# Optimization experiments

Measured on AMD Instinct MI355X. Metric: run time of the kernel, lower is better.

## Reference

```python
import jax, jax.numpy as jnp
import numpy as np

L, H, E, D, FF, V, CTX = 8, 16, 1024, 64, 4096, 2048, 2048
B, T = 4, 1024


def _ln(x, g, b, eps=1e-5):
    mu = x.mean(-1, keepdims=True)
    var = ((x - mu) ** 2).mean(-1, keepdims=True)
    return (x - mu) * jax.lax.rsqrt(var + eps) * g + b


def setup_inputs() -> dict:
    key = jax.random.key(0)
    ks = jax.random.split(key, 12)
    s = 0.02
    return {
        "tokens": jax.random.randint(ks[0], (B, T), 0, V),
        "tok_emb": jax.random.normal(ks[1], (V, E), jnp.float32) * s,
        "pos_emb": jax.random.normal(ks[2], (CTX, E), jnp.float32) * s,
        "Wq": jax.random.normal(ks[3], (L, H, E, D), jnp.float32) * s,
        "Wk": jax.random.normal(ks[4], (L, H, E, D), jnp.float32) * s,
        "Wv": jax.random.normal(ks[5], (L, H, E, D), jnp.float32) * s,
        "Wo": jax.random.normal(ks[6], (L, H * D, E), jnp.float32) * s,
        "bo": jnp.zeros((L, E), jnp.float32),
        "ln1_g": jnp.ones((L, E), jnp.float32),
        "ln1_b": jnp.zeros((L, E), jnp.float32),
        "ln2_g": jnp.ones((L, E), jnp.float32),
        "ln2_b": jnp.zeros((L, E), jnp.float32),
        "W1": jax.random.normal(ks[7], (L, E, FF), jnp.float32) * s,
        "b1": jnp.zeros((L, FF), jnp.float32),
        "W2": jax.random.normal(ks[8], (L, FF, E), jnp.float32) * s,
        "b2": jnp.zeros((L, E), jnp.float32),
        "lnf_g": jnp.ones((E,), jnp.float32),
        "lnf_b": jnp.zeros((E,), jnp.float32),
        "Wlm": jax.random.normal(ks[9], (E, V), jnp.float32) * s,
        "blm": jnp.zeros((V,), jnp.float32),
    }


def reference(tokens, tok_emb, pos_emb, Wq, Wk, Wv, Wo, bo, ln1_g, ln1_b,
              ln2_g, ln2_b, W1, b1, W2, b2, lnf_g, lnf_b, Wlm, blm):
    # NOTE: original indexes pos_embd with token ids (pos_embd(x.int()))
    x = tok_emb[tokens] + pos_emb[tokens]  # [B,T,E]
    t = x.shape[1]
    causal = jnp.tril(jnp.ones((t, t), bool))
    scale = 1.0 / jnp.sqrt(jnp.float32(D))
    for l in range(L):
        x = _ln(x, ln1_g[l], ln1_b[l])
        q = jnp.einsum('bte,hed->bhtd', x, Wq[l])
        k = jnp.einsum('bte,hed->bhtd', x, Wk[l])
        v = jnp.einsum('bte,hed->bhtd', x, Wv[l])
        scores = jnp.einsum('bhtd,bhsd->bhts', q, k) * scale
        scores = jnp.where(causal, scores, -jnp.inf)
        att = jax.nn.softmax(scores, axis=-1)
        o = jnp.einsum('bhts,bhsd->bhtd', att, v)
        o = o.transpose(0, 2, 1, 3).reshape(x.shape[0], t, H * D)
        x = x + o @ Wo[l] + bo[l]
        x = _ln(x, ln2_g[l], ln2_b[l])
        x = x + jax.nn.relu(x @ W1[l] + b1[l]) @ W2[l] + b2[l]
    x = _ln(x, lnf_g, lnf_b)
    return x @ Wlm + blm
```

## Files before the change

### kernel.cpp

```cpp
#include <hip/hip_runtime.h>
#include <hip/hip_bf16.h>

#define LAYERS 8
#define H_ 16
#define E_ 1024
#define D_ 64
#define FF_ 4096
#define V_ 2048
#define B_ 4
#define T_ 1024
#define MTOK (B_*T_)

typedef __bf16 bf16x8_t __attribute__((ext_vector_type(8)));
typedef float f32x4_t __attribute__((ext_vector_type(4)));
typedef __hip_bfloat16 bf16_t;

__device__ __forceinline__ bf16_t f2b(float f) { return __float2bfloat16(f); }

__global__ void embed_kernel(const int* __restrict__ tokens,
                             const float* __restrict__ te,
                             const float* __restrict__ pe,
                             float* __restrict__ x) {
  int row = blockIdx.x;
  int tok = tokens[row];
  const float4* a = (const float4*)(te + (size_t)tok * E_);
  const float4* p = (const float4*)(pe + (size_t)tok * E_);
  float4* o = (float4*)(x + (size_t)row * E_);
  int t = threadIdx.x;
  float4 va = a[t], vp = p[t];
  o[t] = make_float4(va.x + vp.x, va.y + vp.y, va.z + vp.z, va.w + vp.w);
}

__global__ __launch_bounds__(256) void ln_kernel(float* __restrict__ x,
                                                 bf16_t* __restrict__ xb,
                                                 const float* __restrict__ g,
                                                 const float* __restrict__ b) {
  int row = blockIdx.x, tid = threadIdx.x;
  float* xr = x + (size_t)row * E_;
  float4 v = ((const float4*)xr)[tid];
  float s  = v.x + v.y + v.z + v.w;
  float sq = v.x*v.x + v.y*v.y + v.z*v.z + v.w*v.w;
  for (int off = 32; off; off >>= 1) {
    s  += __shfl_xor(s, off, 64);
    sq += __shfl_xor(sq, off, 64);
  }
  __shared__ float2 wred[4];
  if ((tid & 63) == 0) wred[tid >> 6] = make_float2(s, sq);
  __syncthreads();
  float2 w0 = wred[0], w1 = wred[1], w2 = wred[2], w3 = wred[3];
  float S = w0.x + w1.x + w2.x + w3.x, SQ = w0.y + w1.y + w2.y + w3.y;
  float mean = S * (1.0f / E_);
  float var  = SQ * (1.0f / E_) - mean * mean;
  float inv = rsqrtf(var + 1e-5f);
  float4 gv = ((const float4*)g)[tid];
  float4 bv = ((const float4*)b)[tid];
  float o0 = (v.x - mean) * inv * gv.x + bv.x;
  float o1 = (v.y - mean) * inv * gv.y + bv.y;
  float o2 = (v.z - mean) * inv * gv.z + bv.z;
  float o3 = (v.w - mean) * inv * gv.w + bv.w;
  ((float4*)xr)[tid] = make_float4(o0, o1, o2, o3);
  bf16_t* xo = xb + (size_t)row * E_ + tid * 4;
  xo[0] = f2b(o0); xo[1] = f2b(o1); xo[2] = f2b(o2); xo[3] = f2b(o3);
}

__global__ void transpose_kernel(const float* __restrict__ in, bf16_t* __restrict__ out,
                                 int R, int C) {
  __shared__ float tile[32][33];
  int z = blockIdx.z;
  const float* ib = in + (size_t)z * R * C;
  bf16_t* ob = out + (size_t)z * R * C;
  int r0 = blockIdx.y * 32, c0 = blockIdx.x * 32;
  int tx = threadIdx.x, ty = threadIdx.y;
  for (int i = 0; i < 4; i++)
    tile[ty + i * 8][tx] = ib[(size_t)(r0 + ty + i * 8) * C + (c0 + tx)];
  __syncthreads();
  for (int i = 0; i < 4; i++)
    ob[(size_t)(c0 + ty + i * 8) * R + (r0 + tx)] = f2b(tile[tx][ty + i * 8]);
}

#define BK 32

enum { MODE_F32 = 0, MODE_BF16 = 1, MODE_QKV = 2 };

__device__ __forceinline__ void gload16(const bf16_t* g, bf16_t* l) {
  __builtin_amdgcn_global_load_lds((const __attribute__((address_space(1))) void*)g,
                                   (__attribute__((address_space(3))) void*)l, 16, 0, 0);
}

__device__ __forceinline__ int xcd_swz(int flat, int nwg) {
  int q = nwg >> 3, r = nwg & 7;
  int xcd = flat & 7, idx = flat >> 3;
  return (xcd < r ? xcd * (q + 1) : r * (q + 1) + (xcd - r) * q) + idx;
}

template <int BM, int BN, int MODE>
__global__ __launch_bounds__(256) void gemm97_kernel(
    const bf16_t* __restrict__ A, long long sAz, int lda,
    const bf16_t* __restrict__ Bt, long long sBz, int ldb,
    void* __restrict__ C, long long sCz,
    const float* __restrict__ bias,
    const float* __restrict__ resid,
    int M, int N, int K, float alpha, int relu) {
  constexpr int FR = BM / 32, FC = BN / 32;
  constexpr int A_ISS = BM / 64, B_ISS = BN / 64;
  __shared__ __align__(16) bf16_t As[2][BM * BK];
  __shared__ __align__(16) bf16_t Bs[2][BN * BK];
  int tid = threadIdx.x;
  int z = blockIdx.z;
  int nwg = gridDim.x * gridDim.y;
  int flat = xcd_swz(blockIdx.y * gridDim.x + blockIdx.x, nwg);
  int m0 = (flat / gridDim.x) * BM, n0 = (flat % gridDim.x) * BN;
  const bf16_t* Ab = A + (size_t)z * sAz + (size_t)m0 * lda;
  const bf16_t* Bb = Bt + (size_t)z * sBz + (size_t)n0 * ldb;
  int lane = tid & 63, wave = tid >> 6;
  int wr = (wave >> 1) * (BM / 2), wc = (wave & 1) * (BN / 2);
  int lr = lane & 15, lk = (lane >> 4) * 8;
  int srow = tid >> 2;
  int scol = (tid & 3) * 8;

  f32x4_t acc[FR][FC];
  for (int i = 0; i < FR; i++)
    for (int j = 0; j < FC; j++)
      acc[i][j] = (f32x4_t){0.f, 0.f, 0.f, 0.f};

  auto stage = [&](int buf, int k0) {
#pragma unroll
    for (int i = 0; i < A_ISS; i++)
      gload16(Ab + (size_t)(i * 64 + srow) * lda + k0 + scol, &As[buf][i * 2048 + wave * 512]);
#pragma unroll
    for (int i = 0; i < B_ISS; i++)
      gload16(Bb + (size_t)(i * 64 + srow) * ldb + k0 + scol, &Bs[buf][i * 2048 + wave * 512]);
  };

  int nk = K / BK;
  stage(0, 0);
  __syncthreads();
  int cur = 0;
  for (int kt = 0; kt < nk; ++kt) {
    if (kt + 1 < nk) stage(cur ^ 1, (kt + 1) * BK);
    bf16x8_t af[FR], bfv[FC];
#pragma unroll
    for (int i = 0; i < FR; i++)
      af[i] = *(const bf16x8_t*)(&As[cur][(wr + i * 16 + lr) * BK + lk]);
#pragma unroll
    for (int j = 0; j < FC; j++)
      bfv[j] = *(const bf16x8_t*)(&Bs[cur][(wc + j * 16 + lr) * BK + lk]);
#pragma unroll
    for (int i = 0; i < FR; i++)
#pragma unroll
      for (int j = 0; j < FC; j++)
        acc[i][j] = __builtin_amdgcn_mfma_f32_16x16x32_bf16(af[i], bfv[j], acc[i][j], 0, 0, 0);
    __syncthreads();
    cur ^= 1;
  }

#pragma unroll
  for (int i = 0; i < FR; i++)
#pragma unroll
    for (int j = 0; j < FC; j++) {
      f32x4_t v = acc[i][j];
      int n = n0 + wc + j * 16 + lr;
      int mb = m0 + wr + i * 16 + (lane >> 4) * 4;
#pragma unroll
      for (int r = 0; r < 4; r++) {
        int m = mb + r;
        float val = v[r] * alpha;
        if (bias) val += bias[n];
        if (relu) val = fmaxf(val, 0.f);
        if (MODE == MODE_F32) {
          size_t idx = (size_t)z * sCz + (size_t)m * N + n;
          ((float*)C)[idx] = val + (resid ? resid[idx] : 0.f);
        } else if (MODE == MODE_BF16) {
          size_t idx = (size_t)z * sCz + (size_t)m * N + n;
          ((bf16_t*)C)[idx] = f2b(val);
        } else {
          int sect = n >> 10, hd = n & 1023, h = hd >> 6, d = hd & 63;
          int b = m >> 10, t = m & 1023;
          size_t base = (size_t)sect * ((size_t)B_ * H_ * T_ * D_);
          size_t idx = base + ((size_t)(b * H_ + h) << 16) +
                       (sect == 2 ? (size_t)((d << 10) + t) : (size_t)((t << 6) + d));
          ((bf16_t*)C)[idx] = f2b(val);
        }
      }
    }
}

template <int NS>
__global__ __launch_bounds__(256) void splitk_reduce_kernel(const float* __restrict__ p,
                                                            float* __restrict__ x,
                                                            const float* __restrict__ bias) {
  size_t i = (size_t)blockIdx.x * 256 + threadIdx.x;
  float4 acc = ((float4*)x)[i];
  int n4 = (int)(i & (E_ / 4 - 1));
  float4 bv = ((const float4*)bias)[n4];
  acc.x += bv.x; acc.y += bv.y; acc.z += bv.z; acc.w += bv.w;
#pragma unroll
  for (int s = 0; s < NS; s++) {
    float4 a = ((const float4*)p)[i + (size_t)s * ((size_t)MTOK * E_ / 4)];
    acc.x += a.x; acc.y += a.y; acc.z += a.z; acc.w += a.w;
  }
  ((float4*)x)[i] = acc;
}

#define KPAD 72

__global__ __launch_bounds__(256) void flash_kernel(
    const bf16_t* __restrict__ q,
    const bf16_t* __restrict__ kk,
    const bf16_t* __restrict__ vt,
    bf16_t* __restrict__ o) {
  __shared__ __align__(16) bf16_t Ks[64 * KPAD];
  __shared__ __align__(16) bf16_t Vs[64 * KPAD];
  __shared__ __align__(16) bf16_t Ps[4][16 * KPAD];
  int bid = blockIdx.x;
  int qi = 15 - (bid >> 6);
  int bh = bid & 63;
  int b = bh >> 4, h = bh & 15;
  const bf16_t* qb = q + ((size_t)bh << 16);
  const bf16_t* kb = kk + ((size_t)bh << 16);
  const bf16_t* vb = vt + ((size_t)bh << 16);
  int tid = threadIdx.x, lane = tid & 63, wave = tid >> 6;
  int lr = lane & 15, lg = lane >> 4;
  int qbase = qi * 64;

  bf16x8_t qf[2];
  {
    const bf16_t* qrow = qb + (size_t)(qbase + wave * 16 + lr) * D_ + lg * 8;
    qf[0] = *(const bf16x8_t*)(qrow);
    qf[1] = *(const bf16x8_t*)(qrow + 32);
  }

  float m_r[4], l_r[4];
  f32x4_t oc[4];
#pragma unroll
  for (int r = 0; r < 4; r++) { m_r[r] = -1e30f; l_r[r] = 0.f; }
#pragma unroll
  for (int j = 0; j < 4; j++) oc[j] = (f32x4_t){0.f, 0.f, 0.f, 0.f};

  int srow = tid >> 2, scol = (tid & 3) * 16;

  bf16x8_t k0, k1, v0, v1;
  {
    const bf16_t* kg = kb + (size_t)srow * D_ + scol;
    k0 = *(const bf16x8_t*)kg;
    k1 = *(const bf16x8_t*)(kg + 8);
    const bf16_t* vg = vb + (size_t)srow * T_ + scol;
    v0 = *(const bf16x8_t*)vg;
    v1 = *(const bf16x8_t*)(vg + 8);
  }

  for (int s = 0; s <= qi; s++) {
    __syncthreads();
    *(bf16x8_t*)(&Ks[srow * KPAD + scol]) = k0;
    *(bf16x8_t*)(&Ks[srow * KPAD + scol + 8]) = k1;
    *(bf16x8_t*)(&Vs[srow * KPAD + scol]) = v0;
    *(bf16x8_t*)(&Vs[srow * KPAD + scol + 8]) = v1;
    __syncthreads();

    if (s < qi) {
      int kv1 = (s + 1) * 64;
      const bf16_t* kg = kb + (size_t)(kv1 + srow) * D_ + scol;
      k0 = *(const bf16x8_t*)kg;
      k1 = *(const bf16x8_t*)(kg + 8);
      const bf16_t* vg = vb + (size_t)srow * T_ + kv1 + scol;
      v0 = *(const bf16x8_t*)vg;
      v1 = *(const bf16x8_t*)(vg + 8);
    }

    int kv0 = s * 64;
    f32x4_t sc[4];
#pragma unroll
    for (int j = 0; j < 4; j++) {
      f32x4_t a = (f32x4_t){0.f, 0.f, 0.f, 0.f};
      bf16x8_t b0 = *(const bf16x8_t*)(&Ks[(j * 16 + lr) * KPAD + lg * 8]);
      bf16x8_t b1 = *(const bf16x8_t*)(&Ks[(j * 16 + lr) * KPAD + lg * 8 + 32]);
      a = __builtin_amdgcn_mfma_f32_16x16x32_bf16(qf[0], b0, a, 0, 0, 0);
      a = __builtin_amdgcn_mfma_f32_16x16x32_bf16(qf[1], b1, a, 0, 0, 0);
      sc[j] = a;
    }
    if (s == qi) {
#pragma unroll
      for (int j = 0; j < 4; j++)
#pragma unroll
        for (int r = 0; r < 4; r++) {
          int kvp = kv0 + j * 16 + lr;
          int qp  = qbase + wave * 16 + lg * 4 + r;
          sc[j][r] = (kvp <= qp) ? sc[j][r] * 0.125f : -1e30f;
        }
    } else {
#pragma unroll
      for (int j = 0; j < 4; j++)
#pragma unroll
        for (int r = 0; r < 4; r++) sc[j][r] *= 0.125f;
    }

    float ex[4];
#pragma unroll
    for (int r = 0; r < 4; r++) {
      float v = fmaxf(fmaxf(sc[0][r], sc[1][r]), fmaxf(sc[2][r], sc[3][r]));
      v = fmaxf(v, __shfl_xor(v, 1, 64));
      v = fmaxf(v, __shfl_xor(v, 2, 64));
      v = fmaxf(v, __shfl_xor(v, 4, 64));
      v = fmaxf(v, __shfl_xor(v, 8, 64));
      float mn = fmaxf(m_r[r], v);
      ex[r] = __expf(m_r[r] - mn);
      m_r[r] = mn;
      l_r[r] *= ex[r];
    }
#pragma unroll
    for (int j = 0; j < 4; j++)
#pragma unroll
      for (int r = 0; r < 4; r++) {
        float p = __expf(sc[j][r] - m_r[r]);
        l_r[r] += p;
        Ps[wave][(lg * 4 + r) * KPAD + j * 16 + lr] = f2b(p);
      }

#pragma unroll
    for (int j = 0; j < 4; j++)
#pragma unroll
      for (int r = 0; r < 4; r++) oc[j][r] *= ex[r];

    bf16x8_t pa0 = *(const bf16x8_t*)(&Ps[wave][lr * KPAD + lg * 8]);
    bf16x8_t pa1 = *(const bf16x8_t*)(&Ps[wave][lr * KPAD + lg * 8 + 32]);
#pragma unroll
    for (int j = 0; j < 4; j++) {
      bf16x8_t vb0 = *(const bf16x8_t*)(&Vs[(j * 16 + lr) * KPAD + lg * 8]);
      bf16x8_t vb1 = *(const bf16x8_t*)(&Vs[(j * 16 + lr) * KPAD + lg * 8 + 32]);
      oc[j] = __builtin_amdgcn_mfma_f32_16x16x32_bf16(pa0, vb0, oc[j], 0, 0, 0);
      oc[j] = __builtin_amdgcn_mfma_f32_16x16x32_bf16(pa1, vb1, oc[j], 0, 0, 0);
    }
  }

#pragma unroll
  for (int r = 0; r < 4; r++) {
    float v = l_r[r];
    v += __shfl_xor(v, 1, 64);
    v += __shfl_xor(v, 2, 64);
    v += __shfl_xor(v, 4, 64);
    v += __shfl_xor(v, 8, 64);
    l_r[r] = 1.f / v;
  }
  bf16_t* ob = o + ((size_t)(b * T_ + qbase + wave * 16)) * (H_ * D_) + h * D_;
#pragma unroll
  for (int j = 0; j < 4; j++)
#pragma unroll
    for (int r = 0; r < 4; r++) {
      int qrow = lg * 4 + r;
      ob[(size_t)qrow * (H_ * D_) + j * 16 + lr] = f2b(oc[j][r] * l_r[r]);
    }
}

extern "C" void kernel_launch(void* const* d_in, const int* in_sizes, int n_in,
                              void* d_out, int out_size, void* d_ws, size_t ws_size,
                              hipStream_t stream) {
  (void)in_sizes; (void)n_in; (void)out_size;
  const int*   tokens = (const int*)d_in[0];
  const float* tok_emb = (const float*)d_in[1];
  const float* pos_emb = (const float*)d_in[2];
  const float* Wq = (const float*)d_in[3];
  const float* Wk = (const float*)d_in[4];
  const float* Wv = (const float*)d_in[5];
  const float* Wo = (const float*)d_in[6];
  const float* bo = (const float*)d_in[7];
  const float* ln1_g = (const float*)d_in[8];
  const float* ln1_b = (const float*)d_in[9];
  const float* ln2_g = (const float*)d_in[10];
  const float* ln2_b = (const float*)d_in[11];
  const float* W1 = (const float*)d_in[12];
  const float* b1 = (const float*)d_in[13];
  const float* W2 = (const float*)d_in[14];
  const float* b2 = (const float*)d_in[15];
  const float* lnf_g = (const float*)d_in[16];
  const float* lnf_b = (const float*)d_in[17];
  const float* Wlm = (const float*)d_in[18];
  const float* blm = (const float*)d_in[19];

  char* w = (char*)d_ws;
  size_t off = 0;
  auto alloc = [&](size_t bytes) { void* p = (void*)(w + off); off += (bytes + 255) & ~(size_t)255; return p; };
  float*  x    = (float*)alloc((size_t)MTOK * E_ * 4);
  bf16_t* xb   = (bf16_t*)alloc((size_t)MTOK * E_ * 2);
  bf16_t* q    = (bf16_t*)alloc((size_t)B_ * H_ * T_ * D_ * 2);
  bf16_t* kk   = (bf16_t*)alloc((size_t)B_ * H_ * T_ * D_ * 2);
  bf16_t* vt   = (bf16_t*)alloc((size_t)B_ * H_ * T_ * D_ * 2);
  bf16_t* o    = (bf16_t*)alloc((size_t)MTOK * E_ * 2);
  bf16_t* h1   = (bf16_t*)alloc((size_t)MTOK * FF_ * 2);
  bf16_t* WqkvT = (bf16_t*)alloc((size_t)3 * E_ * H_ * D_ * 2);
  bf16_t* WoT  = (bf16_t*)alloc((size_t)E_ * H_ * D_ * 2);
  bf16_t* W1T  = (bf16_t*)alloc((size_t)E_ * FF_ * 2);
  bf16_t* W2T  = (bf16_t*)alloc((size_t)E_ * FF_ * 2);
  bf16_t* WlmT = (bf16_t*)alloc((size_t)E_ * V_ * 2);
  size_t pk_bytes = (size_t)4 * MTOK * E_ * 4;
  bool do_splitk = (ws_size > off + pk_bytes + (1 << 20));
  float* p4 = do_splitk ? (float*)alloc(pk_bytes) : nullptr;

  embed_kernel<<<MTOK, 256, 0, stream>>>(tokens, tok_emb, pos_emb, x);
  transpose_kernel<<<dim3(V_ / 32, E_ / 32, 1), dim3(32, 8), 0, stream>>>(Wlm, WlmT, E_, V_);

  for (int l = 0; l < LAYERS; l++) {
    ln_kernel<<<MTOK, 256, 0, stream>>>(x, xb, ln1_g + l * E_, ln1_b + l * E_);

    transpose_kernel<<<dim3(D_ / 32, E_ / 32, H_), dim3(32, 8), 0, stream>>>(
        Wq + (size_t)l * H_ * E_ * D_, WqkvT, E_, D_);
    transpose_kernel<<<dim3(D_ / 32, E_ / 32, H_), dim3(32, 8), 0, stream>>>(
        Wk + (size_t)l * H_ * E_ * D_, WqkvT + (size_t)E_ * H_ * D_, E_, D_);
    transpose_kernel<<<dim3(D_ / 32, E_ / 32, H_), dim3(32, 8), 0, stream>>>(
        Wv + (size_t)l * H_ * E_ * D_, WqkvT + (size_t)2 * E_ * H_ * D_, E_, D_);
    transpose_kernel<<<dim3(E_ / 32, (H_ * D_) / 32, 1), dim3(32, 8), 0, stream>>>(
        Wo + (size_t)l * H_ * D_ * E_, WoT, H_ * D_, E_);
    transpose_kernel<<<dim3(FF_ / 32, E_ / 32, 1), dim3(32, 8), 0, stream>>>(
        W1 + (size_t)l * E_ * FF_, W1T, E_, FF_);
    transpose_kernel<<<dim3(E_ / 32, FF_ / 32, 1), dim3(32, 8), 0, stream>>>(
        W2 + (size_t)l * FF_ * E_, W2T, FF_, E_);

    gemm97_kernel<128, 128, MODE_QKV><<<dim3(24, 32, 1), 256, 0, stream>>>(
        xb, 0, E_, WqkvT, 0, E_, q, 0, nullptr, nullptr, MTOK, 3 * H_ * D_, E_, 1.f, 0);

    flash_kernel<<<1024, 256, 0, stream>>>(q, kk, vt, o);

    if (do_splitk) {
      gemm97_kernel<128, 128, MODE_F32><<<dim3(8, 32, 2), 256, 0, stream>>>(
          o, 512, H_ * D_, WoT, 512, H_ * D_, p4, (long long)MTOK * E_,
          nullptr, nullptr, MTOK, E_, (H_ * D_) / 2, 1.f, 0);
      splitk_reduce_kernel<2><<<MTOK * E_ / 1024, 256, 0, stream>>>(p4, x, bo + l * E_);
    } else {
      gemm97_kernel<128, 128, MODE_F32><<<dim3(8, 32, 1), 256, 0, stream>>>(
          o, 0, H_ * D_, WoT, 0, H_ * D_, x, 0, bo + l * E_, x, MTOK, E_, H_ * D_, 1.f, 0);
    }

    ln_kernel<<<MTOK, 256, 0, stream>>>(x, xb, ln2_g + l * E_, ln2_b + l * E_);

    gemm97_kernel<128, 128, MODE_BF16><<<dim3(32, 32, 1), 256, 0, stream>>>(
        xb, 0, E_, W1T, 0, E_, h1, 0, b1 + l * FF_, nullptr, MTOK, FF_, E_, 1.f, 1);
    if (do_splitk) {
      gemm97_kernel<128, 128, MODE_F32><<<dim3(8, 32, 4), 256, 0, stream>>>(
          h1, 1024, FF_, W2T, 1024, FF_, p4, (long long)MTOK * E_,
          nullptr, nullptr, MTOK, E_, FF_ / 4, 1.f, 0);
      splitk_reduce_kernel<4><<<MTOK * E_ / 1024, 256, 0, stream>>>(p4, x, b2 + l * E_);
    } else {
      gemm97_kernel<128, 128, MODE_F32><<<dim3(8, 32, 1), 256, 0, stream>>>(
          h1, 0, FF_, W2T, 0, FF_, x, 0, b2 + l * E_, x, MTOK, E_, FF_, 1.f, 0);
    }
  }

  ln_kernel<<<MTOK, 256, 0, stream>>>(x, xb, lnf_g, lnf_b);
  gemm97_kernel<128, 128, MODE_F32><<<dim3(16, 32, 1), 256, 0, stream>>>(
      xb, 0, E_, WlmT, 0, E_, d_out, 0, blm, nullptr, MTOK, V_, E_, 1.f, 0);
}
```

Before: 2.391 ms.

## Replace 128x128 GEMM with 256-row, 512-thread, BK=64 prefetch-two GEMM kernel

Replaces the 128x128/BK=32 GEMM with a kernel using 256-row tiles, 512 threads and BK=64. Operand tiles are stored as 16x32 fragment chunks so each lane reads its MFMA fragment directly. The k-loop keeps two tiles in flight, waits on vmcnt counters instead of a full sync before each compute, and raises wave priority around MFMAs. Split-K is dropped for the Wo projection and reduced from 4 to 2 for W2, which trades fewer reduction passes for fewer blocks (fewer CTAs may underfill the GPU) and larger LDS use per block.

```diff
diff --git a/kernel.cpp b/kernel.cpp
--- a/kernel.cpp
+++ b/kernel.cpp
@@ -78,8 +78,6 @@
     ob[(size_t)(c0 + ty + i * 8) * R + (r0 + tx)] = f2b(tile[tx][ty + i * 8]);
 }
 
-#define BK 32
-
 enum { MODE_F32 = 0, MODE_BF16 = 1, MODE_QKV = 2 };
 
 __device__ __forceinline__ void gload16(const bf16_t* g, bf16_t* l) {
@@ -93,85 +91,104 @@
   return (xcd < r ? xcd * (q + 1) : r * (q + 1) + (xcd - r) * q) + idx;
 }
 
-template <int BM, int BN, int MODE>
-__global__ __launch_bounds__(256) void gemm97_kernel(
-    const bf16_t* __restrict__ A, long long sAz, int lda,
-    const bf16_t* __restrict__ Bt, long long sBz, int ldb,
+template <int BN, int MODE>
+__global__ __launch_bounds__(512, 2) void gemm256_kernel(
+    const bf16_t* __restrict__ A, int lda,
+    const bf16_t* __restrict__ Bt, int ldb,
     void* __restrict__ C, long long sCz,
     const float* __restrict__ bias,
     const float* __restrict__ resid,
-    int M, int N, int K, float alpha, int relu) {
-  constexpr int FR = BM / 32, FC = BN / 32;
-  constexpr int A_ISS = BM / 64, B_ISS = BN / 64;
-  __shared__ __align__(16) bf16_t As[2][BM * BK];
-  __shared__ __align__(16) bf16_t Bs[2][BN * BK];
-  int tid = threadIdx.x;
+    int M, int N, int kspan, int relu) {
+  constexpr int WN = BN / 64;
+  constexpr int WM = 8 / WN;
+  constexpr int MF = 16 / WM;
+  constexpr int ACH = 4;
+  constexpr int BCH = BN / 64;
+  constexpr int LPS = ACH + BCH;
+  __shared__ __align__(16) bf16_t As[2][256 * 64];
+  __shared__ __align__(16) bf16_t Bs[2][BN * 64];
+  int tid = threadIdx.x, lane = tid & 63, wave = tid >> 6;
+  int wm = wave / WN, wn = wave % WN;
   int z = blockIdx.z;
   int nwg = gridDim.x * gridDim.y;
   int flat = xcd_swz(blockIdx.y * gridDim.x + blockIdx.x, nwg);
-  int m0 = (flat / gridDim.x) * BM, n0 = (flat % gridDim.x) * BN;
-  const bf16_t* Ab = A + (size_t)z * sAz + (size_t)m0 * lda;
-  const bf16_t* Bb = Bt + (size_t)z * sBz + (size_t)n0 * ldb;
-  int lane = tid & 63, wave = tid >> 6;
-  int wr = (wave >> 1) * (BM / 2), wc = (wave & 1) * (BN / 2);
-  int lr = lane & 15, lk = (lane >> 4) * 8;
-  int srow = tid >> 2;
-  int scol = (tid & 3) * 8;
-
-  f32x4_t acc[FR][FC];
-  for (int i = 0; i < FR; i++)
-    for (int j = 0; j < FC; j++)
+  int m0 = (flat / gridDim.x) * 256, n0 = (flat % gridDim.x) * BN;
+  const bf16_t* Ab = A + (size_t)m0 * lda + (size_t)z * kspan;
+  const bf16_t* Bb = Bt + (size_t)n0 * ldb + (size_t)z * kspan;
+  int sr = lane & 15, sc = (lane >> 4) * 8;
+
+  f32x4_t acc[MF][4];
+#pragma unroll
+  for (int i = 0; i < MF; i++)
+#pragma unroll
+    for (int j = 0; j < 4; j++)
       acc[i][j] = (f32x4_t){0.f, 0.f, 0.f, 0.f};
 
-  auto stage = [&](int buf, int k0) {
-#pragma unroll
-    for (int i = 0; i < A_ISS; i++)
-      gload16(Ab + (size_t)(i * 64 + srow) * lda + k0 + scol, &As[buf][i * 2048 + wave * 512]);
-#pragma unroll
-    for (int i = 0; i < B_ISS; i++)
-      gload16(Bb + (size_t)(i * 64 + srow) * ldb + k0 + scol, &Bs[buf][i * 2048 + wave * 512]);
+  auto stage = [&](int buf, int kt) {
+    int kg = kt * 64;
+#pragma unroll
+    for (int ch = 0; ch < ACH; ch++) {
+      int sub = wave * ACH + ch;
+      gload16(Ab + (size_t)((sub >> 1) * 16 + sr) * lda + kg + (sub & 1) * 32 + sc,
+              &As[buf][sub * 512]);
+    }
+#pragma unroll
+    for (int ch = 0; ch < BCH; ch++) {
+      int sub = wave * BCH + ch;
+      gload16(Bb + (size_t)((sub >> 1) * 16 + sr) * ldb + kg + (sub & 1) * 32 + sc,
+              &Bs[buf][sub * 512]);
+    }
   };
 
-  int nk = K / BK;
+  int nk = kspan / 64;
   stage(0, 0);
-  __syncthreads();
+  stage(1, 1);
   int cur = 0;
   for (int kt = 0; kt < nk; ++kt) {
-    if (kt + 1 < nk) stage(cur ^ 1, (kt + 1) * BK);
-    bf16x8_t af[FR], bfv[FC];
-#pragma unroll
-    for (int i = 0; i < FR; i++)
-      af[i] = *(const bf16x8_t*)(&As[cur][(wr + i * 16 + lr) * BK + lk]);
-#pragma unroll
-    for (int j = 0; j < FC; j++)
-      bfv[j] = *(const bf16x8_t*)(&Bs[cur][(wc + j * 16 + lr) * BK + lk]);
-#pragma unroll
-    for (int i = 0; i < FR; i++)
-#pragma unroll
-      for (int j = 0; j < FC; j++)
-        acc[i][j] = __builtin_amdgcn_mfma_f32_16x16x32_bf16(af[i], bfv[j], acc[i][j], 0, 0, 0);
-    __syncthreads();
+    if (kt + 1 < nk) { asm volatile("s_waitcnt vmcnt(%0)" :: "n"(LPS) : "memory"); }
+    else             { asm volatile("s_waitcnt vmcnt(0)" ::: "memory"); }
+    __builtin_amdgcn_s_barrier();
+#pragma unroll
+    for (int ks = 0; ks < 2; ks++) {
+      bf16x8_t af[MF], bfv[4];
+#pragma unroll
+      for (int i = 0; i < MF; i++)
+        af[i] = *(const bf16x8_t*)(&As[cur][((wm * MF + i) * 2 + ks) * 512 + lane * 8]);
+#pragma unroll
+      for (int j = 0; j < 4; j++)
+        bfv[j] = *(const bf16x8_t*)(&Bs[cur][((wn * 4 + j) * 2 + ks) * 512 + lane * 8]);
+      __builtin_amdgcn_s_setprio(1);
+#pragma unroll
+      for (int i = 0; i < MF; i++)
+#pragma unroll
+        for (int j = 0; j < 4; j++)
+          acc[i][j] = __builtin_amdgcn_mfma_f32_16x16x32_bf16(af[i], bfv[j], acc[i][j], 0, 0, 0);
+      __builtin_amdgcn_s_setprio(0);
+    }
+    __builtin_amdgcn_sched_barrier(0);
+    __builtin_amdgcn_s_barrier();
+    if (kt + 2 < nk) stage(cur, kt + 2);
     cur ^= 1;
   }
 
 #pragma unroll
-  for (int i = 0; i < FR; i++)
-#pragma unroll
-    for (int j = 0; j < FC; j++) {
+  for (int i = 0; i < MF; i++)
+#pragma unroll
+    for (int j = 0; j < 4; j++) {
       f32x4_t v = acc[i][j];
-      int n = n0 + wc + j * 16 + lr;
-      int mb = m0 + wr + i * 16 + (lane >> 4) * 4;
+      int n = n0 + wn * 64 + j * 16 + (lane & 15);
+      int mb = m0 + wm * (256 / WM) + i * 16 + (lane >> 4) * 4;
 #pragma unroll
       for (int r = 0; r < 4; r++) {
         int m = mb + r;
-        float val = v[r] * alpha;
+        float val = v[r];
         if (bias) val += bias[n];
         if (relu) val = fmaxf(val, 0.f);
         if (MODE == MODE_F32) {
           size_t idx = (size_t)z * sCz + (size_t)m * N + n;
           ((float*)C)[idx] = val + (resid ? resid[idx] : 0.f);
         } else if (MODE == MODE_BF16) {
-          size_t idx = (size_t)z * sCz + (size_t)m * N + n;
+          size_t idx = (size_t)m * N + n;
           ((bf16_t*)C)[idx] = f2b(val);
         } else {
           int sect = n >> 10, hd = n & 1023, h = hd >> 6, d = hd & 63;
@@ -354,7 +371,7 @@
 extern "C" void kernel_launch(void* const* d_in, const int* in_sizes, int n_in,
                               void* d_out, int out_size, void* d_ws, size_t ws_size,
                               hipStream_t stream) {
-  (void)in_sizes; (void)n_in; (void)out_size;
+  (void)in_sizes; (void)n_in; (void)out_size; (void)ws_size;
   const int*   tokens = (const int*)d_in[0];
   const float* tok_emb = (const float*)d_in[1];
   const float* pos_emb = (const float*)d_in[2];
@@ -391,9 +408,7 @@
   bf16_t* W1T  = (bf16_t*)alloc((size_t)E_ * FF_ * 2);
   bf16_t* W2T  = (bf16_t*)alloc((size_t)E_ * FF_ * 2);
   bf16_t* WlmT = (bf16_t*)alloc((size_t)E_ * V_ * 2);
-  size_t pk_bytes = (size_t)4 * MTOK * E_ * 4;
-  bool do_splitk = (ws_size > off + pk_bytes + (1 << 20));
-  float* p4 = do_splitk ? (float*)alloc(pk_bytes) : nullptr;
+  float*  p2   = (float*)alloc((size_t)2 * MTOK * E_ * 4);
 
   embed_kernel<<<MTOK, 256, 0, stream>>>(tokens, tok_emb, pos_emb, x);
   transpose_kernel<<<dim3(V_ / 32, E_ / 32, 1), dim3(32, 8), 0, stream>>>(Wlm, WlmT, E_, V_);
@@ -414,37 +429,24 @@
     transpose_kernel<<<dim3(E_ / 32, FF_ / 32, 1), dim3(32, 8), 0, stream>>>(
         W2 + (size_t)l * FF_ * E_, W2T, FF_, E_);
 
-    gemm97_kernel<128, 128, MODE_QKV><<<dim3(24, 32, 1), 256, 0, stream>>>(
-        xb, 0, E_, WqkvT, 0, E_, q, 0, nullptr, nullptr, MTOK, 3 * H_ * D_, E_, 1.f, 0);
+    gemm256_kernel<256, MODE_QKV><<<dim3(12, 16, 1), 512, 0, stream>>>(
+        xb, E_, WqkvT, E_, q, 0, nullptr, nullptr, MTOK, 3 * H_ * D_, E_, 0);
 
     flash_kernel<<<1024, 256, 0, stream>>>(q, kk, vt, o);
 
-    if (do_splitk) {
-      gemm97_kernel<128, 128, MODE_F32><<<dim3(8, 32, 2), 256, 0, stream>>>(
-          o, 512, H_ * D_, WoT, 512, H_ * D_, p4, (long long)MTOK * E_,
-          nullptr, nullptr, MTOK, E_, (H_ * D_) / 2, 1.f, 0);
-      splitk_reduce_kernel<2><<<MTOK * E_ / 1024, 256, 0, stream>>>(p4, x, bo + l * E_);
-    } else {
-      gemm97_kernel<128, 128, MODE_F32><<<dim3(8, 32, 1), 256, 0, stream>>>(
-          o, 0, H_ * D_, WoT, 0, H_ * D_, x, 0, bo + l * E_, x, MTOK, E_, H_ * D_, 1.f, 0);
-    }
+    gemm256_kernel<128, MODE_F32><<<dim3(8, 16, 1), 512, 0, stream>>>(
+        o, H_ * D_, WoT, H_ * D_, x, 0, bo + l * E_, x, MTOK, E_, H_ * D_, 0);
 
     ln_kernel<<<MTOK, 256, 0, stream>>>(x, xb, ln2_g + l * E_, ln2_b + l * E_);
 
-    gemm97_kernel<128, 128, MODE_BF16><<<dim3(32, 32, 1), 256, 0, stream>>>(
-        xb, 0, E_, W1T, 0, E_, h1, 0, b1 + l * FF_, nullptr, MTOK, FF_, E_, 1.f, 1);
-    if (do_splitk) {
-      gemm97_kernel<128, 128, MODE_F32><<<dim3(8, 32, 4), 256, 0, stream>>>(
-          h1, 1024, FF_, W2T, 1024, FF_, p4, (long long)MTOK * E_,
-          nullptr, nullptr, MTOK, E_, FF_ / 4, 1.f, 0);
-      splitk_reduce_kernel<4><<<MTOK * E_ / 1024, 256, 0, stream>>>(p4, x, b2 + l * E_);
-    } else {
-      gemm97_kernel<128, 128, MODE_F32><<<dim3(8, 32, 1), 256, 0, stream>>>(
-          h1, 0, FF_, W2T, 0, FF_, x, 0, b2 + l * E_, x, MTOK, E_, FF_, 1.f, 0);
-    }
+    gemm256_kernel<256, MODE_BF16><<<dim3(16, 16, 1), 512, 0, stream>>>(
+        xb, E_, W1T, E_, h1, 0, b1 + l * FF_, nullptr, MTOK, FF_, E_, 1);
+    gemm256_kernel<128, MODE_F32><<<dim3(8, 16, 2), 512, 0, stream>>>(
+        h1, FF_, W2T, FF_, p2, (long long)MTOK * E_, nullptr, nullptr, MTOK, E_, FF_ / 2, 0);
+    splitk_reduce_kernel<2><<<MTOK * E_ / 1024, 256, 0, stream>>>(p2, x, b2 + l * E_);
   }
 
   ln_kernel<<<MTOK, 256, 0, stream>>>(x, xb, lnf_g, lnf_b);
-  gemm97_kernel<128, 128, MODE_F32><<<dim3(16, 32, 1), 256, 0, stream>>>(
-      xb, 0, E_, WlmT, 0, E_, d_out, 0, blm, nullptr, MTOK, V_, E_, 1.f, 0);
-}
+  gemm256_kernel<128, MODE_F32><<<dim3(16, 16, 1), 512, 0, stream>>>(
+      xb, E_, WlmT, E_, d_out, 0, blm, nullptr, MTOK, V_, E_, 0);
+}
```

New measurement: 2.889 ms. +20.8%, slower.

## Keep residual stream in bf16 and fuse Wo residual into GEMM epilogue

Applied to the files above, without the earlier changes.

Stores the residual activation stream as bf16 instead of fp32. Layernorm now reads bf16 and writes only a bf16 output, and the Wo projection adds its residual in a new bf16 epilogue, which removes that split-K pass and its reduce kernel. The W2 GEMM now uses 2-way split-K with bf16 partials instead of 4-way fp32. The goal is less memory traffic and fewer launches, at the cost of rounding the residual and the partial sums to bf16, which risks accuracy.

```diff
diff --git a/kernel.cpp b/kernel.cpp
--- a/kernel.cpp
+++ b/kernel.cpp
@@ -12,6 +12,7 @@
 #define MTOK (B_*T_)
 
 typedef __bf16 bf16x8_t __attribute__((ext_vector_type(8)));
+typedef __bf16 bf16x4_t __attribute__((ext_vector_type(4)));
 typedef float f32x4_t __attribute__((ext_vector_type(4)));
 typedef __hip_bfloat16 bf16_t;
 
@@ -20,26 +21,27 @@
 __global__ void embed_kernel(const int* __restrict__ tokens,
                              const float* __restrict__ te,
                              const float* __restrict__ pe,
-                             float* __restrict__ x) {
+                             bf16_t* __restrict__ x) {
   int row = blockIdx.x;
   int tok = tokens[row];
-  const float4* a = (const float4*)(te + (size_t)tok * E_);
-  const float4* p = (const float4*)(pe + (size_t)tok * E_);
-  float4* o = (float4*)(x + (size_t)row * E_);
   int t = threadIdx.x;
-  float4 va = a[t], vp = p[t];
-  o[t] = make_float4(va.x + vp.x, va.y + vp.y, va.z + vp.z, va.w + vp.w);
-}
-
-__global__ __launch_bounds__(256) void ln_kernel(float* __restrict__ x,
-                                                 bf16_t* __restrict__ xb,
+  float4 va = ((const float4*)(te + (size_t)tok * E_))[t];
+  float4 vp = ((const float4*)(pe + (size_t)tok * E_))[t];
+  bf16x4_t o;
+  o[0] = (__bf16)(va.x + vp.x); o[1] = (__bf16)(va.y + vp.y);
+  o[2] = (__bf16)(va.z + vp.z); o[3] = (__bf16)(va.w + vp.w);
+  ((bf16x4_t*)(x + (size_t)row * E_))[t] = o;
+}
+
+__global__ __launch_bounds__(256) void ln_kernel(const bf16_t* __restrict__ xin,
+                                                 bf16_t* __restrict__ xout,
                                                  const float* __restrict__ g,
                                                  const float* __restrict__ b) {
   int row = blockIdx.x, tid = threadIdx.x;
-  float* xr = x + (size_t)row * E_;
-  float4 v = ((const float4*)xr)[tid];
-  float s  = v.x + v.y + v.z + v.w;
-  float sq = v.x*v.x + v.y*v.y + v.z*v.z + v.w*v.w;
+  bf16x4_t v4 = ((const bf16x4_t*)(xin + (size_t)row * E_))[tid];
+  float v0 = (float)v4[0], v1 = (float)v4[1], v2 = (float)v4[2], v3 = (float)v4[3];
+  float s  = v0 + v1 + v2 + v3;
+  float sq = v0*v0 + v1*v1 + v2*v2 + v3*v3;
   for (int off = 32; off; off >>= 1) {
     s  += __shfl_xor(s, off, 64);
     sq += __shfl_xor(sq, off, 64);
@@ -54,13 +56,12 @@
   float inv = rsqrtf(var + 1e-5f);
   float4 gv = ((const float4*)g)[tid];
   float4 bv = ((const float4*)b)[tid];
-  float o0 = (v.x - mean) * inv * gv.x + bv.x;
-  float o1 = (v.y - mean) * inv * gv.y + bv.y;
-  float o2 = (v.z - mean) * inv * gv.z + bv.z;
-  float o3 = (v.w - mean) * inv * gv.w + bv.w;
-  ((float4*)xr)[tid] = make_float4(o0, o1, o2, o3);
-  bf16_t* xo = xb + (size_t)row * E_ + tid * 4;
-  xo[0] = f2b(o0); xo[1] = f2b(o1); xo[2] = f2b(o2); xo[3] = f2b(o3);
+  bf16x4_t o;
+  o[0] = (__bf16)((v0 - mean) * inv * gv.x + bv.x);
+  o[1] = (__bf16)((v1 - mean) * inv * gv.y + bv.y);
+  o[2] = (__bf16)((v2 - mean) * inv * gv.z + bv.z);
+  o[3] = (__bf16)((v3 - mean) * inv * gv.w + bv.w);
+  ((bf16x4_t*)(xout + (size_t)row * E_))[tid] = o;
 }
 
 __global__ void transpose_kernel(const float* __restrict__ in, bf16_t* __restrict__ out,
@@ -80,7 +81,7 @@
 
 #define BK 32
 
-enum { MODE_F32 = 0, MODE_BF16 = 1, MODE_QKV = 2 };
+enum { MODE_F32 = 0, MODE_BF16 = 1, MODE_QKV = 2, MODE_BF16R = 3 };
 
 __device__ __forceinline__ void gload16(const bf16_t* g, bf16_t* l) {
   __builtin_amdgcn_global_load_lds((const __attribute__((address_space(1))) void*)g,
@@ -99,8 +100,8 @@
     const bf16_t* __restrict__ Bt, long long sBz, int ldb,
     void* __restrict__ C, long long sCz,
     const float* __restrict__ bias,
-    const float* __restrict__ resid,
-    int M, int N, int K, float alpha, int relu) {
+    const void* __restrict__ resid,
+    int M, int N, int K, int relu) {
   constexpr int FR = BM / 32, FC = BN / 32;
   constexpr int A_ISS = BM / 64, B_ISS = BN / 64;
   __shared__ __align__(16) bf16_t As[2][BM * BK];
@@ -164,14 +165,18 @@
 #pragma unroll
       for (int r = 0; r < 4; r++) {
         int m = mb + r;
-        float val = v[r] * alpha;
+        float val = v[r];
         if (bias) val += bias[n];
         if (relu) val = fmaxf(val, 0.f);
         if (MODE == MODE_F32) {
           size_t idx = (size_t)z * sCz + (size_t)m * N + n;
-          ((float*)C)[idx] = val + (resid ? resid[idx] : 0.f);
+          ((float*)C)[idx] = val + (resid ? ((const float*)resid)[idx] : 0.f);
         } else if (MODE == MODE_BF16) {
           size_t idx = (size_t)z * sCz + (size_t)m * N + n;
+          ((bf16_t*)C)[idx] = f2b(val);
+        } else if (MODE == MODE_BF16R) {
+          size_t idx = (size_t)m * N + n;
+          val += __bfloat162float(((const bf16_t*)resid)[idx]);
           ((bf16_t*)C)[idx] = f2b(val);
         } else {
           int sect = n >> 10, hd = n & 1023, h = hd >> 6, d = hd & 63;
@@ -186,20 +191,26 @@
 }
 
 template <int NS>
-__global__ __launch_bounds__(256) void splitk_reduce_kernel(const float* __restrict__ p,
-                                                            float* __restrict__ x,
+__global__ __launch_bounds__(256) void splitk_reduce_kernel(const bf16_t* __restrict__ p,
+                                                            const bf16_t* __restrict__ t,
+                                                            bf16_t* __restrict__ r,
                                                             const float* __restrict__ bias) {
   size_t i = (size_t)blockIdx.x * 256 + threadIdx.x;
-  float4 acc = ((float4*)x)[i];
-  int n4 = (int)(i & (E_ / 4 - 1));
-  float4 bv = ((const float4*)bias)[n4];
-  acc.x += bv.x; acc.y += bv.y; acc.z += bv.z; acc.w += bv.w;
+  bf16x8_t tv = ((const bf16x8_t*)t)[i];
+  int base = (int)((i * 8) & (E_ - 1));
+  float acc[8];
+#pragma unroll
+  for (int j = 0; j < 8; j++) acc[j] = (float)tv[j] + bias[base + j];
 #pragma unroll
   for (int s = 0; s < NS; s++) {
-    float4 a = ((const float4*)p)[i + (size_t)s * ((size_t)MTOK * E_ / 4)];
-    acc.x += a.x; acc.y += a.y; acc.z += a.z; acc.w += a.w;
-  }
-  ((float4*)x)[i] = acc;
+    bf16x8_t pv = ((const bf16x8_t*)p)[i + (size_t)s * ((size_t)MTOK * E_ / 8)];
+#pragma unroll
+    for (int j = 0; j < 8; j++) acc[j] += (float)pv[j];
+  }
+  bf16x8_t ov;
+#pragma unroll
+  for (int j = 0; j < 8; j++) ov[j] = (__bf16)acc[j];
+  ((bf16x8_t*)r)[i] = ov;
 }
 
 #define KPAD 72
@@ -354,7 +365,7 @@
 extern "C" void kernel_launch(void* const* d_in, const int* in_sizes, int n_in,
                               void* d_out, int out_size, void* d_ws, size_t ws_size,
                               hipStream_t stream) {
-  (void)in_sizes; (void)n_in; (void)out_size;
+  (void)in_sizes; (void)n_in; (void)out_size; (void)ws_size;
   const int*   tokens = (const int*)d_in[0];
   const float* tok_emb = (const float*)d_in[1];
   const float* pos_emb = (const float*)d_in[2];
@@ -379,8 +390,8 @@
   char* w = (char*)d_ws;
   size_t off = 0;
   auto alloc = [&](size_t bytes) { void* p = (void*)(w + off); off += (bytes + 255) & ~(size_t)255; return p; };
-  float*  x    = (float*)alloc((size_t)MTOK * E_ * 4);
-  bf16_t* xb   = (bf16_t*)alloc((size_t)MTOK * E_ * 2);
+  bf16_t* r    = (bf16_t*)alloc((size_t)MTOK * E_ * 2);
+  bf16_t* t    = (bf16_t*)alloc((size_t)MTOK * E_ * 2);
   bf16_t* q    = (bf16_t*)alloc((size_t)B_ * H_ * T_ * D_ * 2);
   bf16_t* kk   = (bf16_t*)alloc((size_t)B_ * H_ * T_ * D_ * 2);
   bf16_t* vt   = (bf16_t*)alloc((size_t)B_ * H_ * T_ * D_ * 2);
@@ -391,15 +402,13 @@
   bf16_t* W1T  = (bf16_t*)alloc((size_t)E_ * FF_ * 2);
   bf16_t* W2T  = (bf16_t*)alloc((size_t)E_ * FF_ * 2);
   bf16_t* WlmT = (bf16_t*)alloc((size_t)E_ * V_ * 2);
-  size_t pk_bytes = (size_t)4 * MTOK * E_ * 4;
-  bool do_splitk = (ws_size > off + pk_bytes + (1 << 20));
-  float* p4 = do_splitk ? (float*)alloc(pk_bytes) : nullptr;
-
-  embed_kernel<<<MTOK, 256, 0, stream>>>(tokens, tok_emb, pos_emb, x);
+  bf16_t* p2   = (bf16_t*)alloc((size_t)2 * MTOK * E_ * 2);
+
+  embed_kernel<<<MTOK, 256, 0, stream>>>(tokens, tok_emb, pos_emb, r);
   transpose_kernel<<<dim3(V_ / 32, E_ / 32, 1), dim3(32, 8), 0, stream>>>(Wlm, WlmT, E_, V_);
 
   for (int l = 0; l < LAYERS; l++) {
-    ln_kernel<<<MTOK, 256, 0, stream>>>(x, xb, ln1_g + l * E_, ln1_b + l * E_);
+    ln_kernel<<<MTOK, 256, 0, stream>>>(r, t, ln1_g + l * E_, ln1_b + l * E_);
 
     transpose_kernel<<<dim3(D_ / 32, E_ / 32, H_), dim3(32, 8), 0, stream>>>(
         Wq + (size_t)l * H_ * E_ * D_, WqkvT, E_, D_);
@@ -415,36 +424,24 @@
         W2 + (size_t)l * FF_ * E_, W2T, FF_, E_);
 
     gemm97_kernel<128, 128, MODE_QKV><<<dim3(24, 32, 1), 256, 0, stream>>>(
-        xb, 0, E_, WqkvT, 0, E_, q, 0, nullptr, nullptr, MTOK, 3 * H_ * D_, E_, 1.f, 0);
+        t, 0, E_, WqkvT, 0, E_, q, 0, nullptr, nullptr, MTOK, 3 * H_ * D_, E_, 0);
 
     flash_kernel<<<1024, 256, 0, stream>>>(q, kk, vt, o);
 
-    if (do_splitk) {
-      gemm97_kernel<128, 128, MODE_F32><<<dim3(8, 32, 2), 256, 0, stream>>>(
-          o, 512, H_ * D_, WoT, 512, H_ * D_, p4, (long long)MTOK * E_,
-          nullptr, nullptr, MTOK, E_, (H_ * D_) / 2, 1.f, 0);
-      splitk_reduce_kernel<2><<<MTOK * E_ / 1024, 256, 0, stream>>>(p4, x, bo + l * E_);
-    } else {
-      gemm97_kernel<128, 128, MODE_F32><<<dim3(8, 32, 1), 256, 0, stream>>>(
-          o, 0, H_ * D_, WoT, 0, H_ * D_, x, 0, bo + l * E_, x, MTOK, E_, H_ * D_, 1.f, 0);
-    }
-
-    ln_kernel<<<MTOK, 256, 0, stream>>>(x, xb, ln2_g + l * E_, ln2_b + l * E_);
+    gemm97_kernel<128, 128, MODE_BF16R><<<dim3(8, 32, 1), 256, 0, stream>>>(
+        o, 0, H_ * D_, WoT, 0, H_ * D_, r, 0, bo + l * E_, t, MTOK, E_, H_ * D_, 0);
+
+    ln_kernel<<<MTOK, 256, 0, stream>>>(r, t, ln2_g + l * E_, ln2_b + l * E_);
 
     gemm97_kernel<128, 128, MODE_BF16><<<dim3(32, 32, 1), 256, 0, stream>>>(
-        xb, 0, E_, W1T, 0, E_, h1, 0, b1 + l * FF_, nullptr, MTOK, FF_, E_, 1.f, 1);
-    if (do_splitk) {
-      gemm97_kernel<128, 128, MODE_F32><<<dim3(8, 32, 4), 256, 0, stream>>>(
-          h1, 1024, FF_, W2T, 1024, FF_, p4, (long long)MTOK * E_,
-          nullptr, nullptr, MTOK, E_, FF_ / 4, 1.f, 0);
-      splitk_reduce_kernel<4><<<MTOK * E_ / 1024, 256, 0, stream>>>(p4, x, b2 + l * E_);
-    } else {
-      gemm97_kernel<128, 128, MODE_F32><<<dim3(8, 32, 1), 256, 0, stream>>>(
-          h1, 0, FF_, W2T, 0, FF_, x, 0, b2 + l * E_, x, MTOK, E_, FF_, 1.f, 0);
-    }
-  }
-
-  ln_kernel<<<MTOK, 256, 0, stream>>>(x, xb, lnf_g, lnf_b);
+        t, 0, E_, W1T, 0, E_, h1, 0, b1 + l * FF_, nullptr, MTOK, FF_, E_, 1);
+    gemm97_kernel<128, 128, MODE_BF16><<<dim3(8, 32, 2), 256, 0, stream>>>(
+        h1, 2048, FF_, W2T, 2048, FF_, p2, (long long)MTOK * E_,
+        nullptr, nullptr, MTOK, E_, FF_ / 2, 0);
+    splitk_reduce_kernel<2><<<MTOK * E_ / 2048, 256, 0, stream>>>(p2, t, r, b2 + l * E_);
+  }
+
+  ln_kernel<<<MTOK, 256, 0, stream>>>(r, t, lnf_g, lnf_b);
   gemm97_kernel<128, 128, MODE_F32><<<dim3(16, 32, 1), 256, 0, stream>>>(
-      xb, 0, E_, WlmT, 0, E_, d_out, 0, blm, nullptr, MTOK, V_, E_, 1.f, 0);
-}
+      t, 0, E_, WlmT, 0, E_, d_out, 0, blm, nullptr, MTOK, V_, E_, 0);
+}
```

Measured after the change: 2.233 ms. -6.6%, faster.
